# Kernel tuning notes

Measured on AMD Instinct MI355X. Metric: run time of the kernel, lower is better.

Reference implementation:

```python
import jax, jax.numpy as jnp
import numpy as np

B, A, OBS = 4096, 32, 128
E, D, H = 64, 64, 4      # gat_embed_dim, gat_hidden_dim, gat_head_num
R, NA = 256, 16          # rnn_hidden_dim, n_actions


def setup_inputs() -> dict:
    key = jax.random.key(0)
    ks = jax.random.split(key, 20)
    s = 0.05
    return {
        "inputs": jax.random.normal(ks[0], (B, A, OBS), jnp.float32),
        "hidden_state": jax.random.normal(ks[1], (B, A, R), jnp.float32),
        "mask": jax.random.randint(ks[2], (B, A, A), 0, 2, jnp.int32),
        # gat_fc: Linear(OBS -> E)
        "gat_fc_w": jax.random.normal(ks[3], (E, OBS), jnp.float32) * s,
        "gat_fc_b": jnp.zeros((E,), jnp.float32),
        # GAT layer: per-head proj E -> D, attention vectors, output proj H*D -> E
        "W_h": jax.random.normal(ks[4], (H, E, D), jnp.float32) * s,
        "a_src": jax.random.normal(ks[5], (H, D), jnp.float32) * s,
        "a_dst": jax.random.normal(ks[6], (H, D), jnp.float32) * s,
        "W_o": jax.random.normal(ks[7], (H * D, E), jnp.float32) * s,
        "b_o": jnp.zeros((E,), jnp.float32),
        # fc1: Linear(OBS+E -> R)
        "fc1_w": jax.random.normal(ks[8], (R, OBS + E), jnp.float32) * s,
        "fc1_b": jnp.zeros((R,), jnp.float32),
        # GRUCell (torch gate order r,z,n)
        "W_ih": jax.random.normal(ks[9], (3 * R, R), jnp.float32) * s,
        "W_hh": jax.random.normal(ks[10], (3 * R, R), jnp.float32) * s,
        "b_ih": jnp.zeros((3 * R,), jnp.float32),
        "b_hh": jnp.zeros((3 * R,), jnp.float32),
        # LayerNorm(R)
        "ln_g": jnp.ones((R,), jnp.float32),
        "ln_b": jnp.zeros((R,), jnp.float32),
        # fc2: Linear(R -> NA)
        "fc2_w": jax.random.normal(ks[11], (NA, R), jnp.float32) * s,
        "fc2_b": jnp.zeros((NA,), jnp.float32),
    }


def _forward(inputs, hidden_state, mask, gat_fc_w, gat_fc_b, W_h, a_src, a_dst,
             W_o, b_o, fc1_w, fc1_b, W_ih, W_hh, b_ih, b_hh, ln_g, ln_b,
             fc2_w, fc2_b):
    # ---- GAT with adjacency-masked softmax ----
    x = inputs @ gat_fc_w.T + gat_fc_b                       # [B,A,E]
    h = jnp.einsum('bae,hed->bhad', x, W_h)                  # [B,H,A,D]
    s_src = jnp.einsum('bhad,hd->bha', h, a_src)             # [B,H,A]
    s_dst = jnp.einsum('bhad,hd->bha', h, a_dst)             # [B,H,A]
    e = jax.nn.leaky_relu(s_src[..., :, None] + s_dst[..., None, :], 0.2)  # [B,H,A,A]
    e = jnp.where(mask[:, None, :, :] > 0, e, jnp.float32(-1e9))
    alpha = jax.nn.softmax(e, axis=-1)                       # [B,H,A,A]
    agg = jnp.einsum('bhij,bhjd->bhid', alpha, h)            # [B,H,A,D]
    agg = agg.transpose(0, 2, 1, 3).reshape(agg.shape[0], agg.shape[2], -1)  # [B,A,H*D]
    att = agg @ W_o + b_o                                    # [B,A,E]

    # ---- concat + fc1 + ReLU ----
    z_in = jnp.concatenate([inputs, att], axis=-1)           # [B,A,OBS+E]
    b, a, _ = z_in.shape
    z = z_in.reshape(b * a, -1)
    xr = jax.nn.relu(z @ fc1_w.T + fc1_b)                    # [B*A,R]

    # ---- GRUCell ----
    h_in = hidden_state.reshape(b * a, -1)
    gi = xr @ W_ih.T + b_ih
    gh = h_in @ W_hh.T + b_hh
    gi_r, gi_z, gi_n = jnp.split(gi, 3, axis=-1)
    gh_r, gh_z, gh_n = jnp.split(gh, 3, axis=-1)
    r = jax.nn.sigmoid(gi_r + gh_r)
    zt = jax.nn.sigmoid(gi_z + gh_z)
    n = jnp.tanh(gi_n + r * gh_n)
    hh = (1.0 - zt) * n + zt * h_in                          # [B*A,R]

    # ---- LayerNorm + fc2 ----
    mu = jnp.mean(hh, axis=-1, keepdims=True)
    var = jnp.mean(jnp.square(hh - mu), axis=-1, keepdims=True)
    hn = (hh - mu) * jax.lax.rsqrt(var + 1e-5) * ln_g + ln_b
    q = hn @ fc2_w.T + fc2_b                                 # [B*A,NA]
    return q.reshape(b, a, -1), hh.reshape(b, a, -1)


def reference(inputs, hidden_state, mask, gat_fc_w, gat_fc_b, W_h, a_src, a_dst,
              W_o, b_o, fc1_w, fc1_b, W_ih, W_hh, b_ih, b_hh, ln_g, ln_b,
              fc2_w, fc2_b):
    return _forward(inputs, hidden_state, mask, gat_fc_w, gat_fc_b, W_h, a_src,
                    a_dst, W_o, b_o, fc1_w, fc1_b, W_ih, W_hh, b_ih, b_hh,
                    ln_g, ln_b, fc2_w, fc2_b)
```

## Files before the change

### kernel.cpp

```cpp
#include <hip/hip_runtime.h>
#include <hip/hip_bf16.h>

using bf16 = __hip_bfloat16;
typedef __bf16 b8v __attribute__((ext_vector_type(8)));
typedef float  f4v __attribute__((ext_vector_type(4)));

static constexpr int  kB   = 4096;
static constexpr int  kA   = 32;
static constexpr int  kOBS = 128;
static constexpr int  kE   = 64;
static constexpr int  kD   = 64;
static constexpr int  kH   = 4;
static constexpr int  kR   = 256;
static constexpr int  kNA  = 16;
static constexpr long kT   = (long)kB * kA;

__device__ __forceinline__ float ldin(const void* p, long i, int bf) {
    return bf ? (float)((const bf16*)p)[i] : ((const float*)p)[i];
}
__device__ __forceinline__ void stout(void* p, long i, float v, int bf) {
    if (bf) ((bf16*)p)[i] = (bf16)v; else ((float*)p)[i] = v;
}
__device__ __forceinline__ unsigned short f2bu(float f) {
    bf16 b = (bf16)f;
    return __builtin_bit_cast(unsigned short, b);
}

__global__ void k_detect(const void* __restrict__ lng, int* __restrict__ flag)
{
    if (threadIdx.x == 0) {
        unsigned w = *(const unsigned*)lng;
        *flag = (w == 0x3F803F80u) ? 1 : 0;
    }
}

__global__ __launch_bounds__(128) void k0d_whx(
    const void* __restrict__ gw, const void* __restrict__ gb,
    const void* __restrict__ Wh, bf16* __restrict__ Whx,
    float* __restrict__ bh, const int* __restrict__ flag)
{
    const int isbf = *flag;
    const int n = blockIdx.x;
    const int k = threadIdx.x;
    const int head = n >> 6, d = n & 63;
    float acc = 0.f;
    for (int e = 0; e < kE; ++e)
        acc += ldin(gw, e * kOBS + k, isbf) * ldin(Wh, (head * kE + e) * kD + d, isbf);
    Whx[n * 128 + k] = (bf16)acc;
    if (k == 0) {
        float b = 0.f;
        for (int e = 0; e < kE; ++e)
            b += ldin(gb, e, isbf) * ldin(Wh, (head * kE + e) * kD + d, isbf);
        bh[n] = b;
    }
}

__global__ __launch_bounds__(256) void k0e_wcat1(
    const void* __restrict__ Wo, const void* __restrict__ bo,
    const void* __restrict__ fc1w, const void* __restrict__ fc1b,
    bf16* __restrict__ Wcat1, float* __restrict__ biasf, const int* __restrict__ flag)
{
    const int isbf = *flag;
    const int n = blockIdx.x;
    const int j = threadIdx.x;
    float acc = 0.f;
    for (int e = 0; e < kE; ++e)
        acc += ldin(Wo, j * kE + e, isbf) * ldin(fc1w, n * (kOBS + kE) + kOBS + e, isbf);
    Wcat1[n * 384 + 128 + j] = (bf16)acc;
    if (j < 128)
        Wcat1[n * 384 + j] = (bf16)ldin(fc1w, n * (kOBS + kE) + j, isbf);
    if (j == 0) {
        float b = ldin(fc1b, n, isbf);
        for (int e = 0; e < kE; ++e)
            b += ldin(fc1w, n * (kOBS + kE) + kOBS + e, isbf) * ldin(bo, e, isbf);
        biasf[n] = b;
    }
}

__global__ __launch_bounds__(256) void k0b_prep(
    const void* __restrict__ w2, const void* __restrict__ lng,
    const void* __restrict__ lnb, const void* __restrict__ b2,
    float* __restrict__ w2g, float* __restrict__ s2, float* __restrict__ c2,
    const int* __restrict__ flag)
{
    __shared__ float r1[4], r2[4];
    const int isbf = *flag;
    const int na = blockIdx.x;
    const int t  = threadIdx.x;
    float w  = ldin(w2, na * kR + t, isbf);
    float g  = ldin(lng, t, isbf);
    float lb = ldin(lnb, t, isbf);
    float wg = w * g;
    w2g[na * kR + t] = wg;
    float a = wg, b = lb * w;
#pragma unroll
    for (int o = 32; o > 0; o >>= 1) {
        a += __shfl_down(a, o);
        b += __shfl_down(b, o);
    }
    if ((t & 63) == 0) { r1[t >> 6] = a; r2[t >> 6] = b; }
    __syncthreads();
    if (t == 0) {
        s2[na] = r1[0] + r1[1] + r1[2] + r1[3];
        c2[na] = ldin(b2, na, isbf) + r2[0] + r2[1] + r2[2] + r2[3];
    }
}

__global__ __launch_bounds__(256) void k0c_wcat(
    const void* __restrict__ Wih, const void* __restrict__ Whh,
    bf16* __restrict__ Wcat, const int* __restrict__ flag)
{
    const int isbf = *flag;
    long i = (long)blockIdx.x * 256 + threadIdx.x;
    if (i >= 3L * 256 * 512) return;
    const int qq = (int)(i >> 17);
    const int n  = (int)((i >> 9) & 255);
    const int k  = (int)(i & 511);
    const int row = qq * kR + n;
    float v = (k < 256) ? ldin(Wih, row * 256 + k, isbf)
                        : ldin(Whh, row * 256 + (k - 256), isbf);
    Wcat[i] = (bf16)v;
}

__global__ __launch_bounds__(512) void k1_h(
    const void* __restrict__ inp, const bf16* __restrict__ Whx,
    const float* __restrict__ bh, bf16* __restrict__ hbuf,
    const int* __restrict__ flag)
{
    __shared__ __align__(16) unsigned char lds[49152];
    const int  isbf = *flag;
    const int  tid  = threadIdx.x;
    const int  lane = tid & 63;
    const int  l15  = lane & 15, lhi = lane >> 4;
    const int  w    = tid >> 6, wm = w >> 2, q = w & 3;
    const long m0   = (long)blockIdx.x * 128;
    const int  arow = tid >> 3, ak8 = tid & 7;

    auto swz = [](int row, int kb) -> unsigned {
        return (unsigned)(row * 128 + (kb ^ ((row & 7) << 4)));
    };

    f4v acc[4][4];
    {
        f4v zero = {0.f, 0.f, 0.f, 0.f};
#pragma unroll
        for (int i = 0; i < 4; ++i)
#pragma unroll
            for (int j = 0; j < 4; ++j) acc[i][j] = zero;
    }

    b8v ra0, ra1, rb[4];
    float4 rf0a, rf0b, rf1a, rf1b;

    auto loadA = [&](int k0) {
        const int kg = k0 * 64;
        if (isbf) {
            const bf16* ip = (const bf16*)inp;
            ra0 = *reinterpret_cast<const b8v*>(ip + (m0 + arow) * kOBS + kg + ak8 * 8);
            ra1 = *reinterpret_cast<const b8v*>(ip + (m0 + arow + 64) * kOBS + kg + ak8 * 8);
        } else {
            const float* ip = (const float*)inp;
            const float4* p0 = reinterpret_cast<const float4*>(ip + (m0 + arow) * kOBS + kg + ak8 * 8);
            const float4* p1 = reinterpret_cast<const float4*>(ip + (m0 + arow + 64) * kOBS + kg + ak8 * 8);
            rf0a = p0[0]; rf0b = p0[1];
            rf1a = p1[0]; rf1b = p1[1];
        }
    };
    auto loadB = [&](int k0) {
        const int kg = k0 * 64;
#pragma unroll
        for (int j = 0; j < 4; ++j) {
            int c = tid + 512 * j;
            int bq = c >> 9, bn = (c >> 3) & 63, bk8 = c & 7;
            rb[j] = *reinterpret_cast<const b8v*>(Whx + (bq * 64 + bn) * 128 + kg + bk8 * 8);
        }
    };
    auto writeS = [&]() {
        b8v va0, va1;
        if (isbf) { va0 = ra0; va1 = ra1; }
        else {
            union { b8v v; unsigned short u[8]; } t0, t1;
            t0.u[0] = f2bu(rf0a.x); t0.u[1] = f2bu(rf0a.y);
            t0.u[2] = f2bu(rf0a.z); t0.u[3] = f2bu(rf0a.w);
            t0.u[4] = f2bu(rf0b.x); t0.u[5] = f2bu(rf0b.y);
            t0.u[6] = f2bu(rf0b.z); t0.u[7] = f2bu(rf0b.w);
            t1.u[0] = f2bu(rf1a.x); t1.u[1] = f2bu(rf1a.y);
            t1.u[2] = f2bu(rf1a.z); t1.u[3] = f2bu(rf1a.w);
            t1.u[4] = f2bu(rf1b.x); t1.u[5] = f2bu(rf1b.y);
            t1.u[6] = f2bu(rf1b.z); t1.u[7] = f2bu(rf1b.w);
            va0 = t0.v; va1 = t1.v;
        }
        *reinterpret_cast<b8v*>(&lds[swz(arow, ak8 * 16)]) = va0;
        *reinterpret_cast<b8v*>(&lds[swz(arow + 64, ak8 * 16)]) = va1;
#pragma unroll
        for (int j = 0; j < 4; ++j) {
            int c = tid + 512 * j;
            int bq = c >> 9, bn = (c >> 3) & 63, bk8 = c & 7;
            *reinterpret_cast<b8v*>(&lds[16384u + bq * 8192u + swz(bn, bk8 * 16)]) = rb[j];
        }
    };
    auto compute = [&]() {
        const unsigned bbase = 16384u + q * 8192u;
#pragma unroll
        for (int ks = 0; ks < 2; ++ks) {
            const int kb = ks * 64 + lhi * 16;
            b8v bfr[4];
#pragma unroll
            for (int ni = 0; ni < 4; ++ni)
                bfr[ni] = *reinterpret_cast<const b8v*>(&lds[bbase + swz(ni * 16 + l15, kb)]);
#pragma unroll
            for (int mi = 0; mi < 4; ++mi) {
                b8v af = *reinterpret_cast<const b8v*>(&lds[swz(wm * 64 + mi * 16 + l15, kb)]);
#pragma unroll
                for (int ni = 0; ni < 4; ++ni)
                    acc[mi][ni] = __builtin_amdgcn_mfma_f32_16x16x32_bf16(
                        af, bfr[ni], acc[mi][ni], 0, 0, 0);
            }
        }
    };

    loadA(0); loadB(0);
#pragma unroll
    for (int k0 = 0; k0 < 2; ++k0) {
        __syncthreads();
        writeS();
        __syncthreads();
        if (k0 < 1) { loadA(1); loadB(1); }
        compute();
    }

#pragma unroll
    for (int mi = 0; mi < 4; ++mi)
#pragma unroll
        for (int ni = 0; ni < 4; ++ni) {
            const int n = q * 64 + ni * 16 + l15;
#pragma unroll
            for (int r = 0; r < 4; ++r) {
                long m = m0 + wm * 64 + mi * 16 + lhi * 4 + r;
                hbuf[m * 256 + n] = (bf16)(acc[mi][ni][r] + bh[n]);
            }
        }
}

__global__ __launch_bounds__(256) void k12_soft(
    const bf16* __restrict__ hbuf, const void* __restrict__ asrc,
    const void* __restrict__ adst, const int* __restrict__ mask,
    bf16* __restrict__ agg, const int* __restrict__ flag)
{
    __shared__ float hsm[4][32][68];
    __shared__ float al[4][32][33];
    __shared__ float ss[4][32];
    __shared__ float sd[4][32];
    const int  isbf = *flag;
    const int  tid = threadIdx.x, lane = tid & 63, hh = tid >> 6;
    const long b = blockIdx.x;

#pragma unroll
    for (int j = 0; j < 4; ++j) {
        int c = lane + j * 64;
        int t = c >> 3, d8 = c & 7;
        union { b8v v; unsigned short u[8]; } hv;
        hv.v = *reinterpret_cast<const b8v*>(hbuf + (b * 32 + t) * 256 + hh * 64 + d8 * 8);
        float4 f0, f1;
        f0.x = __uint_as_float((unsigned)hv.u[0] << 16);
        f0.y = __uint_as_float((unsigned)hv.u[1] << 16);
        f0.z = __uint_as_float((unsigned)hv.u[2] << 16);
        f0.w = __uint_as_float((unsigned)hv.u[3] << 16);
        f1.x = __uint_as_float((unsigned)hv.u[4] << 16);
        f1.y = __uint_as_float((unsigned)hv.u[5] << 16);
        f1.z = __uint_as_float((unsigned)hv.u[6] << 16);
        f1.w = __uint_as_float((unsigned)hv.u[7] << 16);
        *reinterpret_cast<float4*>(&hsm[hh][t][d8 * 8])     = f0;
        *reinterpret_cast<float4*>(&hsm[hh][t][d8 * 8 + 4]) = f1;
    }
    asm volatile("s_waitcnt lgkmcnt(0)" ::: "memory");

    {
        const int t = lane & 31;
        const void* av = (lane < 32) ? asrc : adst;
        float acc = 0.f;
#pragma unroll
        for (int d4 = 0; d4 < 16; ++d4) {
            float4 hv4 = *reinterpret_cast<const float4*>(&hsm[hh][t][d4 * 4]);
            acc += hv4.x * ldin(av, hh * kD + d4 * 4 + 0, isbf);
            acc += hv4.y * ldin(av, hh * kD + d4 * 4 + 1, isbf);
            acc += hv4.z * ldin(av, hh * kD + d4 * 4 + 2, isbf);
            acc += hv4.w * ldin(av, hh * kD + d4 * 4 + 3, isbf);
        }
        if (lane < 32) ss[hh][t] = acc; else sd[hh][t] = acc;
    }
    asm volatile("s_waitcnt lgkmcnt(0)" ::: "memory");

    {
        const int i = lane & 31, half = lane >> 5;
        const float si = ss[hh][i];
        const int* mrow = mask + (b * 32 + i) * 32 + half * 16;
        float ev[16];
        float m = -3.0e38f;
#pragma unroll
        for (int jj = 0; jj < 16; ++jj) {
            float v = si + sd[hh][half * 16 + jj];
            v = v >= 0.f ? v : 0.2f * v;
            v = (mrow[jj] > 0) ? v : -1e9f;
            ev[jj] = v;
            m = fmaxf(m, v);
        }
        m = fmaxf(m, __shfl_xor(m, 32));
        float s = 0.f;
#pragma unroll
        for (int jj = 0; jj < 16; ++jj) {
            float e = __expf(ev[jj] - m);
            ev[jj] = e; s += e;
        }
        s += __shfl_xor(s, 32);
        const float inv = 1.f / s;
#pragma unroll
        for (int jj = 0; jj < 16; ++jj)
            al[hh][i][half * 16 + jj] = ev[jj] * inv;
    }
    asm volatile("s_waitcnt lgkmcnt(0)" ::: "memory");

#pragma unroll
    for (int g = 0; g < 8; ++g) {
        int c = lane + g * 64;
        int i = c >> 4, d0 = (c & 15) * 4;
        float a0 = 0, a1 = 0, a2 = 0, a3 = 0;
        for (int j = 0; j < 32; ++j) {
            float p = al[hh][i][j];
            float4 hv4 = *reinterpret_cast<const float4*>(&hsm[hh][j][d0]);
            a0 += p * hv4.x; a1 += p * hv4.y; a2 += p * hv4.z; a3 += p * hv4.w;
        }
        ushort4 o;
        o.x = f2bu(a0); o.y = f2bu(a1); o.z = f2bu(a2); o.w = f2bu(a3);
        *reinterpret_cast<ushort4*>(agg + (b * 32 + i) * 256 + hh * 64 + d0) = o;
    }
}

__global__ __launch_bounds__(512) void k3_mfma(
    const void* __restrict__ inp, const bf16* __restrict__ agg,
    const bf16* __restrict__ Wcat1, const float* __restrict__ biasf,
    bf16* __restrict__ xr, const int* __restrict__ flag)
{
    __shared__ __align__(16) unsigned char lds[49152];
    const int  isbf = *flag;
    const int  tid  = threadIdx.x;
    const int  lane = tid & 63;
    const int  l15  = lane & 15, lhi = lane >> 4;
    const int  w    = tid >> 6, wm = w >> 2, q = w & 3;
    const long m0   = (long)blockIdx.x * 128;
    const int  arow = tid >> 3, ak8 = tid & 7;

    auto swz = [](int row, int kb) -> unsigned {
        return (unsigned)(row * 128 + (kb ^ ((row & 7) << 4)));
    };

    f4v acc[4][4];
    {
        f4v zero = {0.f, 0.f, 0.f, 0.f};
#pragma unroll
        for (int i = 0; i < 4; ++i)
#pragma unroll
            for (int j = 0; j < 4; ++j) acc[i][j] = zero;
    }

    b8v ra0, ra1, rb[4];
    float4 rf0a, rf0b, rf1a, rf1b;

    auto loadA = [&](int k0) {
        const int kg = k0 * 64;
        if (kg >= 128) {
            ra0 = *reinterpret_cast<const b8v*>(agg + (m0 + arow) * 256 + (kg - 128) + ak8 * 8);
            ra1 = *reinterpret_cast<const b8v*>(agg + (m0 + arow + 64) * 256 + (kg - 128) + ak8 * 8);
        } else if (isbf) {
            const bf16* ip = (const bf16*)inp;
            ra0 = *reinterpret_cast<const b8v*>(ip + (m0 + arow) * kOBS + kg + ak8 * 8);
            ra1 = *reinterpret_cast<const b8v*>(ip + (m0 + arow + 64) * kOBS + kg + ak8 * 8);
        } else {
            const float* ip = (const float*)inp;
            const float4* p0 = reinterpret_cast<const float4*>(ip + (m0 + arow) * kOBS + kg + ak8 * 8);
            const float4* p1 = reinterpret_cast<const float4*>(ip + (m0 + arow + 64) * kOBS + kg + ak8 * 8);
            rf0a = p0[0]; rf0b = p0[1];
            rf1a = p1[0]; rf1b = p1[1];
        }
    };
    auto loadB = [&](int k0) {
        const int kg = k0 * 64;
#pragma unroll
        for (int j = 0; j < 4; ++j) {
            int c = tid + 512 * j;
            int bq = c >> 9, bn = (c >> 3) & 63, bk8 = c & 7;
            rb[j] = *reinterpret_cast<const b8v*>(Wcat1 + ((long)(bq * 64 + bn)) * 384 + kg + bk8 * 8);
        }
    };
    auto writeS = [&](int k0) {
        const int kg = k0 * 64;
        b8v va0, va1;
        if (kg >= 128 || isbf) { va0 = ra0; va1 = ra1; }
        else {
            union { b8v v; unsigned short u[8]; } t0, t1;
            t0.u[0] = f2bu(rf0a.x); t0.u[1] = f2bu(rf0a.y);
            t0.u[2] = f2bu(rf0a.z); t0.u[3] = f2bu(rf0a.w);
            t0.u[4] = f2bu(rf0b.x); t0.u[5] = f2bu(rf0b.y);
            t0.u[6] = f2bu(rf0b.z); t0.u[7] = f2bu(rf0b.w);
            t1.u[0] = f2bu(rf1a.x); t1.u[1] = f2bu(rf1a.y);
            t1.u[2] = f2bu(rf1a.z); t1.u[3] = f2bu(rf1a.w);
            t1.u[4] = f2bu(rf1b.x); t1.u[5] = f2bu(rf1b.y);
            t1.u[6] = f2bu(rf1b.z); t1.u[7] = f2bu(rf1b.w);
            va0 = t0.v; va1 = t1.v;
        }
        *reinterpret_cast<b8v*>(&lds[swz(arow, ak8 * 16)]) = va0;
        *reinterpret_cast<b8v*>(&lds[swz(arow + 64, ak8 * 16)]) = va1;
#pragma unroll
        for (int j = 0; j < 4; ++j) {
            int c = tid + 512 * j;
            int bq = c >> 9, bn = (c >> 3) & 63, bk8 = c & 7;
            *reinterpret_cast<b8v*>(&lds[16384u + bq * 8192u + swz(bn, bk8 * 16)]) = rb[j];
        }
    };
    auto compute = [&]() {
        const unsigned bbase = 16384u + q * 8192u;
#pragma unroll
        for (int ks = 0; ks < 2; ++ks) {
            const int kb = ks * 64 + lhi * 16;
            b8v bfr[4];
#pragma unroll
            for (int ni = 0; ni < 4; ++ni)
                bfr[ni] = *reinterpret_cast<const b8v*>(&lds[bbase + swz(ni * 16 + l15, kb)]);
#pragma unroll
            for (int mi = 0; mi < 4; ++mi) {
                b8v af = *reinterpret_cast<const b8v*>(&lds[swz(wm * 64 + mi * 16 + l15, kb)]);
#pragma unroll
                for (int ni = 0; ni < 4; ++ni)
                    acc[mi][ni] = __builtin_amdgcn_mfma_f32_16x16x32_bf16(
                        af, bfr[ni], acc[mi][ni], 0, 0, 0);
            }
        }
    };

    loadA(0); loadB(0);
#pragma unroll
    for (int k0 = 0; k0 < 6; ++k0) {
        __syncthreads();
        writeS(k0);
        __syncthreads();
        if (k0 < 5) { loadA(k0 + 1); loadB(k0 + 1); }
        compute();
    }

#pragma unroll
    for (int mi = 0; mi < 4; ++mi)
#pragma unroll
        for (int ni = 0; ni < 4; ++ni) {
            const int n = q * 64 + ni * 16 + l15;
            const float bia = biasf[n];
#pragma unroll
            for (int r = 0; r < 4; ++r) {
                long m = m0 + wm * 64 + mi * 16 + lhi * 4 + r;
                xr[m * 256 + n] = (bf16)fmaxf(acc[mi][ni][r] + bia, 0.f);
            }
        }
}

__global__ __launch_bounds__(512) void k4_gru_mfma(
    const bf16* __restrict__ xr, const void* __restrict__ hprev,
    const bf16* __restrict__ Wcat,
    const void* __restrict__ bih, const void* __restrict__ bhh,
    void* __restrict__ dout, const int* __restrict__ flag)
{
    __shared__ __align__(16) unsigned char lds[40960];
    const int  isbf = *flag;
    const int  tid  = threadIdx.x;
    const int  lane = tid & 63;
    const int  l15  = lane & 15, lhi = lane >> 4;
    const int  w    = tid >> 6, wm = w >> 2, nq = w & 3;
    const long m0   = (long)(blockIdx.x >> 2) * 128;
    const int  n0   = (blockIdx.x & 3) * 64;

    const int arow = tid >> 3, ak8 = tid & 7;

    auto swz = [](int row, int kb) -> unsigned {
        return (unsigned)(row * 128 + (kb ^ ((row & 7) << 4)));
    };

    f4v accr[4], accz[4], acci[4], acch[4];
    {
        f4v zero = {0.f, 0.f, 0.f, 0.f};
#pragma unroll
        for (int i = 0; i < 4; ++i) { accr[i] = zero; accz[i] = zero; acci[i] = zero; acch[i] = zero; }
    }

    b8v ra0, ra1, rb[3];
    float4 rf0a, rf0b, rf1a, rf1b;

    auto loadA = [&](int k0) {
        const int kg = k0 * 64;
        if (kg < 256) {
            ra0 = *reinterpret_cast<const b8v*>(xr + (m0 + arow) * 256 + kg + ak8 * 8);
            ra1 = *reinterpret_cast<const b8v*>(xr + (m0 + arow + 64) * 256 + kg + ak8 * 8);
        } else if (isbf) {
            const bf16* hp = (const bf16*)hprev;
            ra0 = *reinterpret_cast<const b8v*>(hp + (m0 + arow) * 256 + (kg - 256) + ak8 * 8);
            ra1 = *reinterpret_cast<const b8v*>(hp + (m0 + arow + 64) * 256 + (kg - 256) + ak8 * 8);
        } else {
            const float* hp = (const float*)hprev;
            const float4* p0 = reinterpret_cast<const float4*>(hp + (m0 + arow) * 256 + (kg - 256) + ak8 * 8);
            const float4* p1 = reinterpret_cast<const float4*>(hp + (m0 + arow + 64) * 256 + (kg - 256) + ak8 * 8);
            rf0a = p0[0]; rf0b = p0[1];
            rf1a = p1[0]; rf1b = p1[1];
        }
    };
    auto loadB = [&](int k0) {
        const int kg = k0 * 64;
#pragma unroll
        for (int j = 0; j < 3; ++j) {
            int c = tid + 512 * j;
            int bq = c >> 9, bn = (c >> 3) & 63, bk8 = c & 7;
            rb[j] = *reinterpret_cast<const b8v*>(
                Wcat + ((long)(bq * 256 + n0 + bn)) * 512 + kg + bk8 * 8);
        }
    };
    auto writeS = [&](int k0) {
        const int kg = k0 * 64;
        b8v va0, va1;
        if (kg < 256 || isbf) { va0 = ra0; va1 = ra1; }
        else {
            union { b8v v; unsigned short u[8]; } t0, t1;
            t0.u[0] = f2bu(rf0a.x); t0.u[1] = f2bu(rf0a.y);
            t0.u[2] = f2bu(rf0a.z); t0.u[3] = f2bu(rf0a.w);
            t0.u[4] = f2bu(rf0b.x); t0.u[5] = f2bu(rf0b.y);
            t0.u[6] = f2bu(rf0b.z); t0.u[7] = f2bu(rf0b.w);
            t1.u[0] = f2bu(rf1a.x); t1.u[1] = f2bu(rf1a.y);
            t1.u[2] = f2bu(rf1a.z); t1.u[3] = f2bu(rf1a.w);
            t1.u[4] = f2bu(rf1b.x); t1.u[5] = f2bu(rf1b.y);
            t1.u[6] = f2bu(rf1b.z); t1.u[7] = f2bu(rf1b.w);
            va0 = t0.v; va1 = t1.v;
        }
        *reinterpret_cast<b8v*>(&lds[swz(arow, ak8 * 16)]) = va0;
        *reinterpret_cast<b8v*>(&lds[swz(arow + 64, ak8 * 16)]) = va1;
#pragma unroll
        for (int j = 0; j < 3; ++j) {
            int c = tid + 512 * j;
            int bq = c >> 9, bn = (c >> 3) & 63, bk8 = c & 7;
            *reinterpret_cast<b8v*>(&lds[16384u + bq * 8192u + swz(bn, bk8 * 16)]) = rb[j];
        }
    };
    auto compute = [&](int k0) {
#pragma unroll
        for (int ks = 0; ks < 2; ++ks) {
            const int kb = ks * 64 + lhi * 16;
            b8v bfr0 = *reinterpret_cast<const b8v*>(&lds[16384u + 0u * 8192u + swz(nq * 16 + l15, kb)]);
            b8v bfr1 = *reinterpret_cast<const b8v*>(&lds[16384u + 1u * 8192u + swz(nq * 16 + l15, kb)]);
            b8v bfr2 = *reinterpret_cast<const b8v*>(&lds[16384u + 2u * 8192u + swz(nq * 16 + l15, kb)]);
#pragma unroll
            for (int mi = 0; mi < 4; ++mi) {
                b8v af = *reinterpret_cast<const b8v*>(&lds[swz(wm * 64 + mi * 16 + l15, kb)]);
                accr[mi] = __builtin_amdgcn_mfma_f32_16x16x32_bf16(af, bfr0, accr[mi], 0, 0, 0);
                accz[mi] = __builtin_amdgcn_mfma_f32_16x16x32_bf16(af, bfr1, accz[mi], 0, 0, 0);
                if (k0 < 4)
                    acci[mi] = __builtin_amdgcn_mfma_f32_16x16x32_bf16(af, bfr2, acci[mi], 0, 0, 0);
                else
                    acch[mi] = __builtin_amdgcn_mfma_f32_16x16x32_bf16(af, bfr2, acch[mi], 0, 0, 0);
            }
        }
    };

    loadA(0); loadB(0);
#pragma unroll
    for (int k0 = 0; k0 < 8; ++k0) {
        __syncthreads();
        writeS(k0);
        __syncthreads();
        if (k0 < 7) { loadA(k0 + 1); loadB(k0 + 1); }
        compute(k0);
    }

    const int n = n0 + nq * 16 + l15;
    const float br  = ldin(bih, n, isbf)           + ldin(bhh, n, isbf);
    const float bz  = ldin(bih, kR + n, isbf)      + ldin(bhh, kR + n, isbf);
    const float bgi = ldin(bih, 2 * kR + n, isbf);
    const float bgh = ldin(bhh, 2 * kR + n, isbf);
#pragma unroll
    for (int mi = 0; mi < 4; ++mi) {
#pragma unroll
        for (int r = 0; r < 4; ++r) {
            long m = m0 + wm * 64 + mi * 16 + lhi * 4 + r;
            float r_ = 1.f / (1.f + __expf(-(accr[mi][r] + br)));
            float z_ = 1.f / (1.f + __expf(-(accz[mi][r] + bz)));
            float nn = tanhf(acci[mi][r] + bgi + r_ * (acch[mi][r] + bgh));
            float hv = ldin(hprev, m * kR + n, isbf);
            stout(dout, kT * kNA + m * kR + n, (1.f - z_) * nn + z_ * hv, isbf);
        }
    }
}

__global__ __launch_bounds__(256) void k5_lnfc2(
    void* __restrict__ dout, const float* __restrict__ w2g,
    const float* __restrict__ s2, const float* __restrict__ c2,
    const int* __restrict__ flag)
{
    const int isbf = *flag;
    const int tid  = threadIdx.x;
    const int lane = tid & 63;
    const long t   = (long)blockIdx.x * 4 + (tid >> 6);
    const long base = kT * kNA + t * kR + lane * 4;

    float v0, v1, v2, v3;
    if (isbf) {
        const ushort4 u = *reinterpret_cast<const ushort4*>(
            (const unsigned short*)dout + base);
        v0 = __uint_as_float((unsigned)u.x << 16);
        v1 = __uint_as_float((unsigned)u.y << 16);
        v2 = __uint_as_float((unsigned)u.z << 16);
        v3 = __uint_as_float((unsigned)u.w << 16);
    } else {
        const float4 f = *reinterpret_cast<const float4*>((const float*)dout + base);
        v0 = f.x; v1 = f.y; v2 = f.z; v3 = f.w;
    }

    float s = v0 + v1 + v2 + v3;
#pragma unroll
    for (int o = 32; o > 0; o >>= 1) s += __shfl_xor(s, o);
    const float mu = s * (1.f / 256.f);
    float d0 = v0 - mu, d1 = v1 - mu, d2 = v2 - mu, d3 = v3 - mu;
    float vs = d0 * d0 + d1 * d1 + d2 * d2 + d3 * d3;
#pragma unroll
    for (int o = 32; o > 0; o >>= 1) vs += __shfl_xor(vs, o);
    const float rstd = rsqrtf(vs * (1.f / 256.f) + 1e-5f);

    const float4* wp = reinterpret_cast<const float4*>(w2g);
    float p[16];
#pragma unroll
    for (int na = 0; na < 16; ++na) {
        float4 w = wp[na * 64 + lane];
        p[na] = v0 * w.x + v1 * w.y + v2 * w.z + v3 * w.w;
    }
#pragma unroll
    for (int na = 0; na < 16; ++na) {
#pragma unroll
        for (int o = 32; o > 0; o >>= 1) p[na] += __shfl_xor(p[na], o);
    }
    if (lane < kNA) {
        float qv = rstd * (p[lane] - mu * s2[lane]) + c2[lane];
        stout(dout, t * kNA + lane, qv, isbf);
    }
}

extern "C" void kernel_launch(void* const* d_in, const int* in_sizes, int n_in,
                              void* d_out, int out_size, void* d_ws, size_t ws_size,
                              hipStream_t stream)
{
    const void* inp   = d_in[0];
    const void* hprev = d_in[1];
    const int*  mask  = (const int*)d_in[2];
    const void* gw    = d_in[3];
    const void* gb    = d_in[4];
    const void* Wh    = d_in[5];
    const void* asrc  = d_in[6];
    const void* adst  = d_in[7];
    const void* Wo    = d_in[8];
    const void* bo    = d_in[9];
    const void* fc1w  = d_in[10];
    const void* fc1b  = d_in[11];
    const void* Wih   = d_in[12];
    const void* Whh   = d_in[13];
    const void* bih   = d_in[14];
    const void* bhh   = d_in[15];
    const void* lng   = d_in[16];
    const void* lnb   = d_in[17];
    const void* w2    = d_in[18];
    const void* b2    = d_in[19];

    bf16*  agg   = (bf16*)d_ws;
    bf16*  xr    = agg + kT * 256;
    bf16*  Wcat1 = xr + kT * 256;
    float* biasf = (float*)((char*)Wcat1 + 262144);
    int*   flag  = (int*)(biasf + 256);
    bf16*  hbuf  = xr;
    bf16*  Whx   = agg;
    float* bh    = (float*)(agg + 32768);
    bf16*  Wcat  = agg;
    float* w2g   = (float*)(agg + 4 * 256 * 512);
    float* s2    = w2g + 4096;
    float* c2    = s2 + 16;

    k_detect<<<1, 64, 0, stream>>>(lng, flag);
    k0d_whx<<<256, 128, 0, stream>>>(gw, gb, Wh, Whx, bh, flag);
    k0e_wcat1<<<256, 256, 0, stream>>>(Wo, bo, fc1w, fc1b, Wcat1, biasf, flag);
    k1_h<<<kT / 128, 512, 0, stream>>>(inp, Whx, bh, hbuf, flag);
    k12_soft<<<kB, 256, 0, stream>>>(hbuf, asrc, adst, mask, agg, flag);
    k3_mfma<<<kT / 128, 512, 0, stream>>>(inp, agg, Wcat1, biasf, xr, flag);
    k0c_wcat<<<1536, 256, 0, stream>>>(Wih, Whh, Wcat, flag);
    k0b_prep<<<16, 256, 0, stream>>>(w2, lng, lnb, b2, w2g, s2, c2, flag);
    k4_gru_mfma<<<(kT / 128) * 4, 512, 0, stream>>>(xr, hprev, Wcat, bih, bhh, d_out, flag);
    k5_lnfc2<<<kT / 4, 256, 0, stream>>>(d_out, w2g, s2, c2, flag);
}
```

Measured before the change: 899.6 us.

## Use MFMA for LayerNorm+fc2 and remap GRU blocks across XCDs

Replaces the wave-per-row shuffle-reduction LayerNorm+fc2 kernel with a 128-row-per-block kernel. It computes row mean and variance with a one-pass sum and sum of squares, then does the 256x16 projection with bf16 MFMA, using LN-folded weights stored as bf16 in LDS. The GRU kernel's block index is also permuted so that consecutive physical blocks map to spread-out virtual tiles, likely to improve L2 locality across XCDs. The fp32 path now rounds activations to bf16 before the MFMA, and the one-pass variance is slightly less accurate.

```diff
diff --git a/kernel.cpp b/kernel.cpp
--- a/kernel.cpp
+++ b/kernel.cpp
@@ -80,7 +80,7 @@
 __global__ __launch_bounds__(256) void k0b_prep(
     const void* __restrict__ w2, const void* __restrict__ lng,
     const void* __restrict__ lnb, const void* __restrict__ b2,
-    float* __restrict__ w2g, float* __restrict__ s2, float* __restrict__ c2,
+    bf16* __restrict__ w2gb, float* __restrict__ s2, float* __restrict__ c2,
     const int* __restrict__ flag)
 {
     __shared__ float r1[4], r2[4];
@@ -91,7 +91,7 @@
     float g  = ldin(lng, t, isbf);
     float lb = ldin(lnb, t, isbf);
     float wg = w * g;
-    w2g[na * kR + t] = wg;
+    w2gb[na * kR + t] = (bf16)wg;
     float a = wg, b = lb * w;
 #pragma unroll
     for (int o = 32; o > 0; o >>= 1) {
@@ -473,8 +473,10 @@
     const int  lane = tid & 63;
     const int  l15  = lane & 15, lhi = lane >> 4;
     const int  w    = tid >> 6, wm = w >> 2, nq = w & 3;
-    const long m0   = (long)(blockIdx.x >> 2) * 128;
-    const int  n0   = (blockIdx.x & 3) * 64;
+    const int  phys = blockIdx.x;
+    const int  virt = (phys >> 3) + ((phys & 7) << 9);
+    const long m0   = (long)(virt >> 2) * 128;
+    const int  n0   = (virt & 3) * 64;
 
     const int arow = tid >> 3, ak8 = tid & 7;
 
@@ -593,55 +595,89 @@
     }
 }
 
-__global__ __launch_bounds__(256) void k5_lnfc2(
-    void* __restrict__ dout, const float* __restrict__ w2g,
+__global__ __launch_bounds__(512) void k5_mfma(
+    void* __restrict__ dout, const bf16* __restrict__ w2gb,
     const float* __restrict__ s2, const float* __restrict__ c2,
     const int* __restrict__ flag)
 {
-    const int isbf = *flag;
-    const int tid  = threadIdx.x;
-    const int lane = tid & 63;
-    const long t   = (long)blockIdx.x * 4 + (tid >> 6);
-    const long base = kT * kNA + t * kR + lane * 4;
-
-    float v0, v1, v2, v3;
-    if (isbf) {
-        const ushort4 u = *reinterpret_cast<const ushort4*>(
-            (const unsigned short*)dout + base);
-        v0 = __uint_as_float((unsigned)u.x << 16);
-        v1 = __uint_as_float((unsigned)u.y << 16);
-        v2 = __uint_as_float((unsigned)u.z << 16);
-        v3 = __uint_as_float((unsigned)u.w << 16);
-    } else {
-        const float4 f = *reinterpret_cast<const float4*>((const float*)dout + base);
-        v0 = f.x; v1 = f.y; v2 = f.z; v3 = f.w;
-    }
-
-    float s = v0 + v1 + v2 + v3;
-#pragma unroll
-    for (int o = 32; o > 0; o >>= 1) s += __shfl_xor(s, o);
-    const float mu = s * (1.f / 256.f);
-    float d0 = v0 - mu, d1 = v1 - mu, d2 = v2 - mu, d3 = v3 - mu;
-    float vs = d0 * d0 + d1 * d1 + d2 * d2 + d3 * d3;
-#pragma unroll
-    for (int o = 32; o > 0; o >>= 1) vs += __shfl_xor(vs, o);
-    const float rstd = rsqrtf(vs * (1.f / 256.f) + 1e-5f);
-
-    const float4* wp = reinterpret_cast<const float4*>(w2g);
-    float p[16];
-#pragma unroll
-    for (int na = 0; na < 16; ++na) {
-        float4 w = wp[na * 64 + lane];
-        p[na] = v0 * w.x + v1 * w.y + v2 * w.z + v3 * w.w;
-    }
-#pragma unroll
-    for (int na = 0; na < 16; ++na) {
-#pragma unroll
-        for (int o = 32; o > 0; o >>= 1) p[na] += __shfl_xor(p[na], o);
-    }
-    if (lane < kNA) {
-        float qv = rstd * (p[lane] - mu * s2[lane]) + c2[lane];
-        stout(dout, t * kNA + lane, qv, isbf);
+    __shared__ __align__(16) bf16 wsh[16][264];
+    __shared__ float stats[8][16][2];
+    const int  isbf = *flag;
+    const int  tid  = threadIdx.x;
+    const int  lane = tid & 63;
+    const int  l15  = lane & 15, lhi = lane >> 4;
+    const int  w    = tid >> 6;
+    const long m0   = (long)blockIdx.x * 128;
+
+    {
+        int na = tid >> 5, ck = tid & 31;
+        *reinterpret_cast<b8v*>(&wsh[na][ck * 8]) =
+            *reinterpret_cast<const b8v*>(w2gb + na * 256 + ck * 8);
+    }
+
+    {
+        const long rowm = m0 + w * 16 + l15;
+        float sum = 0.f, ssq = 0.f;
+        if (isbf) {
+            const unsigned short* hp = (const unsigned short*)dout + kT * kNA + rowm * 256 + lhi * 64;
+#pragma unroll
+            for (int j = 0; j < 8; ++j) {
+                b8v v = *reinterpret_cast<const b8v*>(hp + j * 8);
+#pragma unroll
+                for (int e = 0; e < 8; ++e) {
+                    float f = __uint_as_float((unsigned)__builtin_bit_cast(unsigned short, v[e]) << 16);
+                    sum += f; ssq += f * f;
+                }
+            }
+        } else {
+            const float* hp = (const float*)dout + kT * kNA + rowm * 256 + lhi * 64;
+#pragma unroll
+            for (int j = 0; j < 16; ++j) {
+                float4 f = *reinterpret_cast<const float4*>(hp + j * 4);
+                sum += f.x + f.y + f.z + f.w;
+                ssq += f.x * f.x + f.y * f.y + f.z * f.z + f.w * f.w;
+            }
+        }
+        sum += __shfl_xor(sum, 16); sum += __shfl_xor(sum, 32);
+        ssq += __shfl_xor(ssq, 16); ssq += __shfl_xor(ssq, 32);
+        float mu = sum * (1.f / 256.f);
+        float var = ssq * (1.f / 256.f) - mu * mu;
+        if (lhi == 0) {
+            stats[w][l15][0] = mu;
+            stats[w][l15][1] = rsqrtf(var + 1e-5f);
+        }
+    }
+    __syncthreads();
+
+    f4v acc = {0.f, 0.f, 0.f, 0.f};
+    const long arow = m0 + w * 16 + l15;
+#pragma unroll
+    for (int kb = 0; kb < 8; ++kb) {
+        b8v af;
+        if (isbf) {
+            af = *reinterpret_cast<const b8v*>(
+                (const unsigned short*)dout + kT * kNA + arow * 256 + kb * 32 + lhi * 8);
+        } else {
+            const float* p = (const float*)dout + kT * kNA + arow * 256 + kb * 32 + lhi * 8;
+            float4 f0 = *reinterpret_cast<const float4*>(p);
+            float4 f1 = *reinterpret_cast<const float4*>(p + 4);
+            union { b8v v; unsigned short u[8]; } t;
+            t.u[0] = f2bu(f0.x); t.u[1] = f2bu(f0.y); t.u[2] = f2bu(f0.z); t.u[3] = f2bu(f0.w);
+            t.u[4] = f2bu(f1.x); t.u[5] = f2bu(f1.y); t.u[6] = f2bu(f1.z); t.u[7] = f2bu(f1.w);
+            af = t.v;
+        }
+        b8v bf = *reinterpret_cast<const b8v*>(&wsh[l15][kb * 32 + lhi * 8]);
+        acc = __builtin_amdgcn_mfma_f32_16x16x32_bf16(af, bf, acc, 0, 0, 0);
+    }
+
+    const float s2v = s2[l15], c2v = c2[l15];
+#pragma unroll
+    for (int r = 0; r < 4; ++r) {
+        int rr = lhi * 4 + r;
+        long m = m0 + w * 16 + rr;
+        float mu = stats[w][rr][0], rstd = stats[w][rr][1];
+        float qv = rstd * (acc[r] - mu * s2v) + c2v;
+        stout(dout, m * kNA + l15, qv, isbf);
     }
 }
 
@@ -679,9 +715,9 @@
     bf16*  Whx   = agg;
     float* bh    = (float*)(agg + 32768);
     bf16*  Wcat  = agg;
-    float* w2g   = (float*)(agg + 4 * 256 * 512);
-    float* s2    = w2g + 4096;
+    float* s2    = (float*)(agg + 4 * 256 * 512);
     float* c2    = s2 + 16;
+    bf16*  w2gb  = (bf16*)(c2 + 16);
 
     k_detect<<<1, 64, 0, stream>>>(lng, flag);
     k0d_whx<<<256, 128, 0, stream>>>(gw, gb, Wh, Whx, bh, flag);
@@ -690,7 +726,7 @@
     k12_soft<<<kB, 256, 0, stream>>>(hbuf, asrc, adst, mask, agg, flag);
     k3_mfma<<<kT / 128, 512, 0, stream>>>(inp, agg, Wcat1, biasf, xr, flag);
     k0c_wcat<<<1536, 256, 0, stream>>>(Wih, Whh, Wcat, flag);
-    k0b_prep<<<16, 256, 0, stream>>>(w2, lng, lnb, b2, w2g, s2, c2, flag);
+    k0b_prep<<<16, 256, 0, stream>>>(w2, lng, lnb, b2, w2gb, s2, c2, flag);
     k4_gru_mfma<<<(kT / 128) * 4, 512, 0, stream>>>(xr, hprev, Wcat, bih, bhh, d_out, flag);
-    k5_lnfc2<<<kT / 4, 256, 0, stream>>>(d_out, w2g, s2, c2, flag);
-}
+    k5_mfma<<<kT / 128, 512, 0, stream>>>(d_out, w2gb, s2, c2, flag);
+}
```

Result: faster. 807.3 us (-10.3%).
